# Kernel tuning notes

Measured on AMD Instinct MI355X. Metric: run time of the kernel, lower is better.

## Reference

```python
import jax, jax.numpy as jnp
import numpy as np

N_NODES = 100000
N_EDGES = 1600000
NFEAT, NHID, NCLASS = 512, 128, 64


def setup_inputs() -> dict:
    key = jax.random.key(0)
    ks = jax.random.split(key, 8)
    y = jax.random.normal(ks[0], (N_NODES, NFEAT), dtype=jnp.float32)
    src = jax.random.randint(ks[1], (N_EDGES,), 0, N_NODES, dtype=jnp.int64)
    dst = jax.random.randint(ks[2], (N_EDGES,), 0, N_NODES, dtype=jnp.int64)
    edge_w = jax.random.uniform(ks[3], (N_EDGES,), dtype=jnp.float32)
    # GraphConvolution params (Glorot-ish scale)
    W1 = jax.random.normal(ks[4], (NFEAT, NHID), dtype=jnp.float32) / np.sqrt(NFEAT)
    b1 = jax.random.normal(ks[5], (NHID,), dtype=jnp.float32) * 0.01
    W2 = jax.random.normal(ks[6], (NHID, NCLASS), dtype=jnp.float32) / np.sqrt(NHID)
    b2 = jax.random.normal(ks[7], (NCLASS,), dtype=jnp.float32) * 0.01
    return {"y": y, "src": src, "dst": dst, "edge_w": edge_w,
            "W1": W1, "b1": b1, "W2": W2, "b2": b2}


def _graph_conv(x, W, b, src, dst, edge_w, n_nodes):
    # support = x @ W ; out = spmm(adj, support) + b  (adj in COO form)
    support = x @ W                                   # [N, out_dim]
    msgs = support[src] * edge_w[:, None]             # [E, out_dim] gather
    agg = jax.ops.segment_sum(msgs, dst, num_segments=n_nodes)  # scatter-add
    return agg + b


def reference(y, src, dst, edge_w, W1, b1, W2, b2):
    h = jax.nn.leaky_relu(_graph_conv(y, W1, b1, src, dst, edge_w, N_NODES),
                          negative_slope=0.01)        # F.leaky_relu default
    y_embedding = h
    logits = _graph_conv(h, W2, b2, src, dst, edge_w, N_NODES)
    return (jax.nn.softmax(logits, axis=1), y_embedding)
```

## Files before the change

kernel.cpp:

```cpp
#include <hip/hip_runtime.h>
#include <hip/hip_fp16.h>

#define NN 100000
#define NE 1600000
#define F0 512
#define F1 128
#define F2 64

typedef short bf16x8 __attribute__((ext_vector_type(8)));
typedef float f32x4  __attribute__((ext_vector_type(4)));

static __device__ __forceinline__ unsigned short f2bf(float f) {
    unsigned int u = __float_as_uint(f);
    return (unsigned short)((u + 0x7FFFu + ((u >> 16) & 1u)) >> 16);
}

static __device__ __forceinline__ unsigned short f2h(float f) {
    __half h = __float2half(f);
    return *(unsigned short*)&h;
}

static __device__ __forceinline__ float2 h2f2(unsigned int u) {
    __half2 h = *(__half2*)&u;
    return __half22float2(h);
}

__global__ __launch_bounds__(256)
void wt_kernel(const float* __restrict__ W1, const float* __restrict__ W2,
               unsigned short* __restrict__ W1t, unsigned short* __restrict__ W2t,
               int* __restrict__ cnt, int grid_threads)
{
    int i = blockIdx.x * 256 + threadIdx.x;
    if (i < F0 * F1) {
        int n = i / F0, k = i % F0;
        W1t[i] = f2bf(W1[k * F1 + n]);
    } else {
        int j = i - F0 * F1;
        if (j < F1 * F2) {
            int n = j / F1, k = j % F1;
            W2t[j] = f2bf(W2[k * F2 + n]);
        }
    }
    for (int z = i; z < NN + 256; z += grid_threads) cnt[z] = 0;
}

template<int BM, int BN, int BK, int TN, bool FILL>
__global__ __launch_bounds__(256)
void gemm_edge_kernel(const float* __restrict__ A, const unsigned short* __restrict__ Bt,
                      unsigned short* __restrict__ C, int M, int K, int N,
                      int row_base, int gemm_blocks,
                      const int* __restrict__ src, const int* __restrict__ dst,
                      const float* __restrict__ ew, const int* __restrict__ rowptr,
                      const int* __restrict__ bsum,
                      int* __restrict__ cnt, int* __restrict__ rank,
                      int2* __restrict__ rec, int ne)
{
    constexpr int LDA = BK + 8;
    constexpr int LDB = BK + 8;
    __shared__ unsigned short As[BM * LDA];
    __shared__ unsigned short Bs[BN * LDB];

    if ((int)blockIdx.x >= gemm_blocks) {
        int e = ((int)blockIdx.x - gemm_blocks) * 256 + threadIdx.x;
        if (e < ne) {
            if constexpr (!FILL) {
                rank[e] = atomicAdd(&cnt[dst[e]], 1);
            } else {
                int d = dst[e];
                int pos = rowptr[d] + bsum[d >> 8] + rank[e];
                rec[pos] = make_int2(src[e], __float_as_int(ew[e]));
            }
        }
        return;
    }

    const int tid  = threadIdx.x;
    const int wave = tid >> 6;
    const int lane = tid & 63;
    const int lr   = lane & 15;
    const int quad = lane >> 4;
    const int row0 = row_base + (int)blockIdx.x * BM;

    f32x4 acc[2][TN];
#pragma unroll
    for (int i = 0; i < 2; i++)
#pragma unroll
        for (int j = 0; j < TN; j++) acc[i][j] = (f32x4)0.f;

    for (int k0 = 0; k0 < K; k0 += BK) {
#pragma unroll
        for (int l = tid; l < BM * (BK / 4); l += 256) {
            int m  = l / (BK / 4);
            int kq = l % (BK / 4);
            int rg = row0 + m; if (rg >= M) rg = M - 1;
            float4 v = *(const float4*)(A + (long long)rg * K + k0 + kq * 4);
            ushort4 b = make_ushort4(f2bf(v.x), f2bf(v.y), f2bf(v.z), f2bf(v.w));
            *(ushort4*)(&As[m * LDA + kq * 4]) = b;
        }
#pragma unroll
        for (int l = tid; l < BN * (BK / 8); l += 256) {
            int n  = l / (BK / 8);
            int ko = l % (BK / 8);
            uint4 v = *(const uint4*)(Bt + (long long)n * K + k0 + ko * 8);
            *(uint4*)(&Bs[n * LDB + ko * 8]) = v;
        }
        __syncthreads();

#pragma unroll
        for (int kk = 0; kk < BK; kk += 32) {
            bf16x8 a[2], b[TN];
#pragma unroll
            for (int tm = 0; tm < 2; tm++)
                a[tm] = *(const bf16x8*)(&As[(wave * 32 + tm * 16 + lr) * LDA + kk + quad * 8]);
#pragma unroll
            for (int tn = 0; tn < TN; tn++)
                b[tn] = *(const bf16x8*)(&Bs[(tn * 16 + lr) * LDB + kk + quad * 8]);
#pragma unroll
            for (int tm = 0; tm < 2; tm++)
#pragma unroll
                for (int tn = 0; tn < TN; tn++)
                    acc[tm][tn] = __builtin_amdgcn_mfma_f32_16x16x32_bf16(
                        a[tm], b[tn], acc[tm][tn], 0, 0, 0);
        }
        __syncthreads();
    }

#pragma unroll
    for (int tm = 0; tm < 2; tm++) {
#pragma unroll
        for (int r = 0; r < 4; r++) {
            int row = row0 + wave * 32 + tm * 16 + quad * 4 + r;
            if (row < M) {
#pragma unroll
                for (int tn = 0; tn < TN; tn++)
                    C[(long long)row * N + tn * 16 + lr] = f2h(acc[tm][tn][r]);
            }
        }
    }
}

__global__ __launch_bounds__(256)
void scan1_kernel(const int* __restrict__ cnt, int* __restrict__ rowptr,
                  int* __restrict__ bsum, int n)
{
    __shared__ int s[256];
    int t = threadIdx.x;
    int i = blockIdx.x * 256 + t;
    int v = (i <= n) ? cnt[i] : 0;
    s[t] = v;
    __syncthreads();
#pragma unroll
    for (int off = 1; off < 256; off <<= 1) {
        int x = (t >= off) ? s[t - off] : 0;
        __syncthreads();
        s[t] += x;
        __syncthreads();
    }
    if (i <= n) rowptr[i] = s[t] - v;
    if (t == 255) bsum[blockIdx.x] = s[255];
}

__global__ __launch_bounds__(512)
void scan2_kernel(int* __restrict__ bsum, int nb)
{
    __shared__ int s[512];
    int t = threadIdx.x;
    int v = (t < nb) ? bsum[t] : 0;
    s[t] = v;
    __syncthreads();
#pragma unroll
    for (int off = 1; off < 512; off <<= 1) {
        int x = (t >= off) ? s[t - off] : 0;
        __syncthreads();
        s[t] += x;
        __syncthreads();
    }
    if (t < nb) bsum[t] = s[t] - v;
}

__global__ __launch_bounds__(256)
void agg1_fused_kernel(const unsigned int* __restrict__ sup, const int2* __restrict__ rec,
                       const int* __restrict__ rowptr, const int* __restrict__ bsum,
                       const float* __restrict__ b1,
                       const unsigned short* __restrict__ W2t,
                       float* __restrict__ h, unsigned short* __restrict__ sup2, int n)
{
    constexpr int LDH = F1 + 8;
    __shared__ unsigned short hsb[16 * LDH];

    const int tid  = threadIdx.x;
    const int w    = tid >> 6;
    const int lane = tid & 63;
    const int half = lane >> 5;
    const int sl   = lane & 31;
    const int base = blockIdx.x * 16;

    float4 bb = *(const float4*)(b1 + sl * 4);

#pragma unroll
    for (int it = 0; it < 2; it++) {
        int row  = w * 4 + it * 2 + half;
        int node = base + row;
        float4 acc = make_float4(0.f, 0.f, 0.f, 0.f);
        if (node < n) {
            int j   = rowptr[node]     + bsum[node >> 8];
            int end = rowptr[node + 1] + bsum[(node + 1) >> 8];
            for (; j + 8 <= end; j += 8) {
                int2 r[8];
#pragma unroll
                for (int u = 0; u < 8; u++) r[u] = rec[j + u];
                uint2 uu[8];
#pragma unroll
                for (int u = 0; u < 8; u++)
                    uu[u] = *(const uint2*)(&sup[(long long)r[u].x * 64 + sl * 2]);
#pragma unroll
                for (int u = 0; u < 8; u++) {
                    float2 fa = h2f2(uu[u].x);
                    float2 fb = h2f2(uu[u].y);
                    float  ww = __int_as_float(r[u].y);
                    acc.x = fmaf(fa.x, ww, acc.x);
                    acc.y = fmaf(fa.y, ww, acc.y);
                    acc.z = fmaf(fb.x, ww, acc.z);
                    acc.w = fmaf(fb.y, ww, acc.w);
                }
            }
            for (; j < end; j++) {
                int2 r0 = rec[j];
                uint2 u0 = *(const uint2*)(&sup[(long long)r0.x * 64 + sl * 2]);
                float2 fa = h2f2(u0.x);
                float2 fb = h2f2(u0.y);
                float  ww = __int_as_float(r0.y);
                acc.x = fmaf(fa.x, ww, acc.x);
                acc.y = fmaf(fa.y, ww, acc.y);
                acc.z = fmaf(fb.x, ww, acc.z);
                acc.w = fmaf(fb.y, ww, acc.w);
            }
            acc.x += bb.x;  acc.y += bb.y;  acc.z += bb.z;  acc.w += bb.w;
            acc.x = acc.x > 0.f ? acc.x : 0.01f * acc.x;
            acc.y = acc.y > 0.f ? acc.y : 0.01f * acc.y;
            acc.z = acc.z > 0.f ? acc.z : 0.01f * acc.z;
            acc.w = acc.w > 0.f ? acc.w : 0.01f * acc.w;
            *(float4*)(h + (long long)node * 128 + sl * 4) = acc;
        }
        ushort4 hv = (node < n)
            ? make_ushort4(f2bf(acc.x), f2bf(acc.y), f2bf(acc.z), f2bf(acc.w))
            : make_ushort4(0, 0, 0, 0);
        *(ushort4*)(&hsb[row * LDH + sl * 4]) = hv;
    }
    __syncthreads();

    const int lr   = lane & 15;
    const int quad = lane >> 4;
    f32x4 acc2 = (f32x4)0.f;
#pragma unroll
    for (int kk = 0; kk < F1; kk += 32) {
        bf16x8 a = *(const bf16x8*)(&hsb[lr * LDH + kk + quad * 8]);
        bf16x8 b = *(const bf16x8*)(W2t + (w * 16 + lr) * F1 + kk + quad * 8);
        acc2 = __builtin_amdgcn_mfma_f32_16x16x32_bf16(a, b, acc2, 0, 0, 0);
    }
#pragma unroll
    for (int r = 0; r < 4; r++) {
        int node = base + quad * 4 + r;
        if (node < n)
            sup2[(long long)node * 64 + w * 16 + lr] = f2h(acc2[r]);
    }
}

__global__ __launch_bounds__(256)
void agg2_kernel(const unsigned short* __restrict__ sup, const int2* __restrict__ rec,
                 const int* __restrict__ rowptr, const int* __restrict__ bsum,
                 const float* __restrict__ b2, float* __restrict__ out, int n)
{
    const int lane = threadIdx.x & 63;
    const int half = lane >> 5;
    const int sl   = lane & 31;
    const int node = blockIdx.x * 8 + (threadIdx.x >> 6) * 2 + half;
    if (node >= n) return;

    int j   = rowptr[node]     + bsum[node >> 8];
    int end = rowptr[node + 1] + bsum[(node + 1) >> 8];
    float2 acc = make_float2(0.f, 0.f);

    for (; j + 8 <= end; j += 8) {
        int2 r[8];
#pragma unroll
        for (int u = 0; u < 8; u++) r[u] = rec[j + u];
        unsigned int uu[8];
#pragma unroll
        for (int u = 0; u < 8; u++)
            uu[u] = *(const unsigned int*)(&sup[(long long)r[u].x * 64 + sl * 2]);
#pragma unroll
        for (int u = 0; u < 8; u++) {
            float2 f = h2f2(uu[u]);
            float  ww = __int_as_float(r[u].y);
            acc.x = fmaf(f.x, ww, acc.x);
            acc.y = fmaf(f.y, ww, acc.y);
        }
    }
    for (; j < end; j++) {
        int2 r0 = rec[j];
        unsigned int u0 = *(const unsigned int*)(&sup[(long long)r0.x * 64 + sl * 2]);
        float2 f = h2f2(u0);
        float  ww = __int_as_float(r0.y);
        acc.x = fmaf(f.x, ww, acc.x);
        acc.y = fmaf(f.y, ww, acc.y);
    }

    float2 bv = *(const float2*)(b2 + sl * 2);
    float2 v  = make_float2(acc.x + bv.x, acc.y + bv.y);
    float m = fmaxf(v.x, v.y);
#pragma unroll
    for (int off = 16; off; off >>= 1) m = fmaxf(m, __shfl_xor(m, off, 64));
    float2 e = make_float2(__expf(v.x - m), __expf(v.y - m));
    float s = e.x + e.y;
#pragma unroll
    for (int off = 16; off; off >>= 1) s += __shfl_xor(s, off, 64);
    float inv = 1.f / s;
    *(float2*)(out + (long long)node * 64 + sl * 2) = make_float2(e.x * inv, e.y * inv);
}

extern "C" void kernel_launch(void* const* d_in, const int* in_sizes, int n_in,
                              void* d_out, int out_size, void* d_ws, size_t ws_size,
                              hipStream_t stream)
{
    const float* y   = (const float*)d_in[0];
    const int*   src = (const int*)  d_in[1];
    const int*   dst = (const int*)  d_in[2];
    const float* ew  = (const float*)d_in[3];
    const float* W1  = (const float*)d_in[4];
    const float* b1  = (const float*)d_in[5];
    const float* W2  = (const float*)d_in[6];
    const float* b2  = (const float*)d_in[7];

    float* out     = (float*)d_out;
    float* softout = out;
    float* h       = out + (size_t)NN * F2;

    char* ws = (char*)d_ws;
    size_t o = 0;
    auto alloc = [&](size_t bytes) -> void* {
        void* p = ws + o;
        o = (o + bytes + 255) & ~(size_t)255;
        return p;
    };
    unsigned short* sup  = (unsigned short*)alloc((size_t)NN * F1 * 2);
    unsigned short* sup2 = (unsigned short*)alloc((size_t)NN * F2 * 2);
    int2*           rec  = (int2*)          alloc((size_t)NE * 8);
    int*            rank = (int*)           alloc((size_t)NE * 4);
    int*            rowptr = (int*)         alloc((size_t)(NN + 2) * 4);
    int*            cnt  = (int*)           alloc((size_t)(NN + 256) * 4);
    int*            bsum = (int*)           alloc(512 * 4);
    unsigned short* W1t  = (unsigned short*)alloc((size_t)F0 * F1 * 2);
    unsigned short* W2t  = (unsigned short*)alloc((size_t)F1 * F2 * 2);

    const int NB = (NN + 255) / 256;
    const int GB = (NN + 127) / 128;
    const int GA = 312;
    const int EB = (NE + 255) / 256;

    wt_kernel<<<NB, 256, 0, stream>>>(W1, W2, W1t, W2t, cnt, NB * 256);

    gemm_edge_kernel<128, 128, 64, 8, false><<<GA + EB, 256, 0, stream>>>(
        y, W1t, sup, NN, F0, F1, 0, GA,
        src, dst, ew, rowptr, bsum, cnt, rank, rec, NE);

    scan1_kernel<<<NB, 256, 0, stream>>>(cnt, rowptr, bsum, NN);
    scan2_kernel<<<1, 512, 0, stream>>>(bsum, NB);

    gemm_edge_kernel<128, 128, 64, 8, true><<<(GB - GA) + EB, 256, 0, stream>>>(
        y, W1t, sup, NN, F0, F1, GA * 128, GB - GA,
        src, dst, ew, rowptr, bsum, cnt, rank, rec, NE);

    agg1_fused_kernel<<<(NN + 15) / 16, 256, 0, stream>>>(
        (const unsigned int*)sup, rec, rowptr, bsum, b1, W2t, h, sup2, NN);

    agg2_kernel<<<(NN + 7) / 8, 256, 0, stream>>>(
        sup2, rec, rowptr, bsum, b2, softout, NN);
}
```

Before: 553.2 us.

## Overlap scan with GEMM tiles and use nontemporal loads/stores for streaming data

Moves 64 GEMM row-tiles into the scan1 launch so the prefix-scan blocks share a grid with GEMM blocks, which fills the otherwise small scan launch with useful work and shrinks the final GEMM+fill launch. The GEMM body is factored into a shared device helper. Edge records, rank, the h output and the softmax output now go through nontemporal loads and stores, so these single-use streams are meant to stay out of cache and leave room for the gathered support rows. The combined kernel's shared-memory footprint is the GEMM's, which may limit occupancy for the scan blocks.

```diff
diff --git a/kernel.cpp b/kernel.cpp
--- a/kernel.cpp
+++ b/kernel.cpp
@@ -9,6 +9,7 @@
 
 typedef short bf16x8 __attribute__((ext_vector_type(8)));
 typedef float f32x4  __attribute__((ext_vector_type(4)));
+typedef float f32x2  __attribute__((ext_vector_type(2)));
 
 static __device__ __forceinline__ unsigned short f2bf(float f) {
     unsigned int u = __float_as_uint(f);
@@ -42,6 +43,79 @@
         }
     }
     for (int z = i; z < NN + 256; z += grid_threads) cnt[z] = 0;
+}
+
+template<int BM, int BN, int BK, int TN>
+static __device__ __forceinline__
+void gemm_tile(unsigned short* As, unsigned short* Bs,
+               const float* __restrict__ A, const unsigned short* __restrict__ Bt,
+               unsigned short* __restrict__ C, int M, int K, int N, int row0)
+{
+    constexpr int LDA = BK + 8;
+    constexpr int LDB = BK + 8;
+
+    const int tid  = threadIdx.x;
+    const int wave = tid >> 6;
+    const int lane = tid & 63;
+    const int lr   = lane & 15;
+    const int quad = lane >> 4;
+
+    f32x4 acc[2][TN];
+#pragma unroll
+    for (int i = 0; i < 2; i++)
+#pragma unroll
+        for (int j = 0; j < TN; j++) acc[i][j] = (f32x4)0.f;
+
+    for (int k0 = 0; k0 < K; k0 += BK) {
+#pragma unroll
+        for (int l = tid; l < BM * (BK / 4); l += 256) {
+            int m  = l / (BK / 4);
+            int kq = l % (BK / 4);
+            int rg = row0 + m; if (rg >= M) rg = M - 1;
+            float4 v = *(const float4*)(A + (long long)rg * K + k0 + kq * 4);
+            ushort4 b = make_ushort4(f2bf(v.x), f2bf(v.y), f2bf(v.z), f2bf(v.w));
+            *(ushort4*)(&As[m * LDA + kq * 4]) = b;
+        }
+#pragma unroll
+        for (int l = tid; l < BN * (BK / 8); l += 256) {
+            int n  = l / (BK / 8);
+            int ko = l % (BK / 8);
+            uint4 v = *(const uint4*)(Bt + (long long)n * K + k0 + ko * 8);
+            *(uint4*)(&Bs[n * LDB + ko * 8]) = v;
+        }
+        __syncthreads();
+
+#pragma unroll
+        for (int kk = 0; kk < BK; kk += 32) {
+            bf16x8 a[2], b[TN];
+#pragma unroll
+            for (int tm = 0; tm < 2; tm++)
+                a[tm] = *(const bf16x8*)(&As[(wave * 32 + tm * 16 + lr) * LDA + kk + quad * 8]);
+#pragma unroll
+            for (int tn = 0; tn < TN; tn++)
+                b[tn] = *(const bf16x8*)(&Bs[(tn * 16 + lr) * LDB + kk + quad * 8]);
+#pragma unroll
+            for (int tm = 0; tm < 2; tm++)
+#pragma unroll
+                for (int tn = 0; tn < TN; tn++)
+                    acc[tm][tn] = __builtin_amdgcn_mfma_f32_16x16x32_bf16(
+                        a[tm], b[tn], acc[tm][tn], 0, 0, 0);
+        }
+        __syncthreads();
+    }
+
+#pragma unroll
+    for (int tm = 0; tm < 2; tm++) {
+#pragma unroll
+        for (int r = 0; r < 4; r++) {
+            int row = row0 + wave * 32 + tm * 16 + quad * 4 + r;
+            if (row < M) {
+#pragma unroll
+                for (int tn = 0; tn < TN; tn++)
+                    C[(long long)row * N + tn * 16 + lr] = f2h(acc[tm][tn][r]);
+            }
+        }
+    }
 }
 
 template<int BM, int BN, int BK, int TN, bool FILL>
@@ -55,109 +129,60 @@
                       int* __restrict__ cnt, int* __restrict__ rank,
                       int2* __restrict__ rec, int ne)
 {
-    constexpr int LDA = BK + 8;
-    constexpr int LDB = BK + 8;
-    __shared__ unsigned short As[BM * LDA];
-    __shared__ unsigned short Bs[BN * LDB];
+    __shared__ unsigned short As[BM * (BK + 8)];
+    __shared__ unsigned short Bs[BN * (BK + 8)];
 
     if ((int)blockIdx.x >= gemm_blocks) {
         int e = ((int)blockIdx.x - gemm_blocks) * 256 + threadIdx.x;
         if (e < ne) {
             if constexpr (!FILL) {
-                rank[e] = atomicAdd(&cnt[dst[e]], 1);
+                int rk = atomicAdd(&cnt[dst[e]], 1);
+                __builtin_nontemporal_store(rk, &rank[e]);
             } else {
                 int d = dst[e];
-                int pos = rowptr[d] + bsum[d >> 8] + rank[e];
+                int rk = __builtin_nontemporal_load(&rank[e]);
+                int pos = rowptr[d] + bsum[d >> 8] + rk;
                 rec[pos] = make_int2(src[e], __float_as_int(ew[e]));
             }
         }
         return;
     }
-
-    const int tid  = threadIdx.x;
-    const int wave = tid >> 6;
-    const int lane = tid & 63;
-    const int lr   = lane & 15;
-    const int quad = lane >> 4;
-    const int row0 = row_base + (int)blockIdx.x * BM;
-
-    f32x4 acc[2][TN];
-#pragma unroll
-    for (int i = 0; i < 2; i++)
-#pragma unroll
-        for (int j = 0; j < TN; j++) acc[i][j] = (f32x4)0.f;
-
-    for (int k0 = 0; k0 < K; k0 += BK) {
-#pragma unroll
-        for (int l = tid; l < BM * (BK / 4); l += 256) {
-            int m  = l / (BK / 4);
-            int kq = l % (BK / 4);
-            int rg = row0 + m; if (rg >= M) rg = M - 1;
-            float4 v = *(const float4*)(A + (long long)rg * K + k0 + kq * 4);
-            ushort4 b = make_ushort4(f2bf(v.x), f2bf(v.y), f2bf(v.z), f2bf(v.w));
-            *(ushort4*)(&As[m * LDA + kq * 4]) = b;
-        }
-#pragma unroll
-        for (int l = tid; l < BN * (BK / 8); l += 256) {
-            int n  = l / (BK / 8);
-            int ko = l % (BK / 8);
-            uint4 v = *(const uint4*)(Bt + (long long)n * K + k0 + ko * 8);
-            *(uint4*)(&Bs[n * LDB + ko * 8]) = v;
-        }
+    gemm_tile<BM, BN, BK, TN>(As, Bs, A, Bt, C, M, K, N,
+                              row_base + (int)blockIdx.x * BM);
+}
+
+template<int BM, int BN, int BK, int TN>
+__global__ __launch_bounds__(256)
+void gemm_scan_kernel(const float* __restrict__ A, const unsigned short* __restrict__ Bt,
+                      unsigned short* __restrict__ C, int M, int K, int N,
+                      int row_base, int gemm_blocks,
+                      const int* __restrict__ cnt, int* __restrict__ rowptr,
+                      int* __restrict__ bsum, int n)
+{
+    __shared__ unsigned short As[BM * (BK + 8)];
+    __shared__ unsigned short Bs[BN * (BK + 8)];
+
+    if ((int)blockIdx.x >= gemm_blocks) {
+        __shared__ int s[256];
+        int blk = (int)blockIdx.x - gemm_blocks;
+        int t = threadIdx.x;
+        int i = blk * 256 + t;
+        int v = (i <= n) ? cnt[i] : 0;
+        s[t] = v;
         __syncthreads();
-
-#pragma unroll
-        for (int kk = 0; kk < BK; kk += 32) {
-            bf16x8 a[2], b[TN];
-#pragma unroll
-            for (int tm = 0; tm < 2; tm++)
-                a[tm] = *(const bf16x8*)(&As[(wave * 32 + tm * 16 + lr) * LDA + kk + quad * 8]);
-#pragma unroll
-            for (int tn = 0; tn < TN; tn++)
-                b[tn] = *(const bf16x8*)(&Bs[(tn * 16 + lr) * LDB + kk + quad * 8]);
-#pragma unroll
-            for (int tm = 0; tm < 2; tm++)
-#pragma unroll
-                for (int tn = 0; tn < TN; tn++)
-                    acc[tm][tn] = __builtin_amdgcn_mfma_f32_16x16x32_bf16(
-                        a[tm], b[tn], acc[tm][tn], 0, 0, 0);
-        }
-        __syncthreads();
-    }
-
-#pragma unroll
-    for (int tm = 0; tm < 2; tm++) {
-#pragma unroll
-        for (int r = 0; r < 4; r++) {
-            int row = row0 + wave * 32 + tm * 16 + quad * 4 + r;
-            if (row < M) {
-#pragma unroll
-                for (int tn = 0; tn < TN; tn++)
-                    C[(long long)row * N + tn * 16 + lr] = f2h(acc[tm][tn][r]);
-            }
-        }
-    }
-}
-
-__global__ __launch_bounds__(256)
-void scan1_kernel(const int* __restrict__ cnt, int* __restrict__ rowptr,
-                  int* __restrict__ bsum, int n)
-{
-    __shared__ int s[256];
-    int t = threadIdx.x;
-    int i = blockIdx.x * 256 + t;
-    int v = (i <= n) ? cnt[i] : 0;
-    s[t] = v;
-    __syncthreads();
-#pragma unroll
-    for (int off = 1; off < 256; off <<= 1) {
-        int x = (t >= off) ? s[t - off] : 0;
-        __syncthreads();
-        s[t] += x;
-        __syncthreads();
-    }
-    if (i <= n) rowptr[i] = s[t] - v;
-    if (t == 255) bsum[blockIdx.x] = s[255];
+#pragma unroll
+        for (int off = 1; off < 256; off <<= 1) {
+            int x = (t >= off) ? s[t - off] : 0;
+            __syncthreads();
+            s[t] += x;
+            __syncthreads();
+        }
+        if (i <= n) rowptr[i] = s[t] - v;
+        if (t == 255) bsum[blk] = s[255];
+        return;
+    }
+    gemm_tile<BM, BN, BK, TN>(As, Bs, A, Bt, C, M, K, N,
+                              row_base + (int)blockIdx.x * BM);
 }
 
 __global__ __launch_bounds__(512)
@@ -188,6 +213,8 @@
     constexpr int LDH = F1 + 8;
     __shared__ unsigned short hsb[16 * LDH];
 
+    const long long* recq = (const long long*)rec;
+
     const int tid  = threadIdx.x;
     const int w    = tid >> 6;
     const int lane = tid & 63;
@@ -195,29 +222,29 @@
     const int sl   = lane & 31;
     const int base = blockIdx.x * 16;
 
-    float4 bb = *(const float4*)(b1 + sl * 4);
+    f32x4 bb = *(const f32x4*)(b1 + sl * 4);
 
 #pragma unroll
     for (int it = 0; it < 2; it++) {
         int row  = w * 4 + it * 2 + half;
         int node = base + row;
-        float4 acc = make_float4(0.f, 0.f, 0.f, 0.f);
+        f32x4 acc = (f32x4)0.f;
         if (node < n) {
             int j   = rowptr[node]     + bsum[node >> 8];
             int end = rowptr[node + 1] + bsum[(node + 1) >> 8];
             for (; j + 8 <= end; j += 8) {
-                int2 r[8];
-#pragma unroll
-                for (int u = 0; u < 8; u++) r[u] = rec[j + u];
+                long long r[8];
+#pragma unroll
+                for (int u = 0; u < 8; u++) r[u] = __builtin_nontemporal_load(&recq[j + u]);
                 uint2 uu[8];
 #pragma unroll
                 for (int u = 0; u < 8; u++)
-                    uu[u] = *(const uint2*)(&sup[(long long)r[u].x * 64 + sl * 2]);
+                    uu[u] = *(const uint2*)(&sup[(long long)(int)r[u] * 64 + sl * 2]);
 #pragma unroll
                 for (int u = 0; u < 8; u++) {
                     float2 fa = h2f2(uu[u].x);
                     float2 fb = h2f2(uu[u].y);
-                    float  ww = __int_as_float(r[u].y);
+                    float  ww = __int_as_float((int)(r[u] >> 32));
                     acc.x = fmaf(fa.x, ww, acc.x);
                     acc.y = fmaf(fa.y, ww, acc.y);
                     acc.z = fmaf(fb.x, ww, acc.z);
@@ -225,11 +252,11 @@
                 }
             }
             for (; j < end; j++) {
-                int2 r0 = rec[j];
-                uint2 u0 = *(const uint2*)(&sup[(long long)r0.x * 64 + sl * 2]);
+                long long r0 = __builtin_nontemporal_load(&recq[j]);
+                uint2 u0 = *(const uint2*)(&sup[(long long)(int)r0 * 64 + sl * 2]);
                 float2 fa = h2f2(u0.x);
                 float2 fb = h2f2(u0.y);
-                float  ww = __int_as_float(r0.y);
+                float  ww = __int_as_float((int)(r0 >> 32));
                 acc.x = fmaf(fa.x, ww, acc.x);
                 acc.y = fmaf(fa.y, ww, acc.y);
                 acc.z = fmaf(fb.x, ww, acc.z);
@@ -240,7 +267,7 @@
             acc.y = acc.y > 0.f ? acc.y : 0.01f * acc.y;
             acc.z = acc.z > 0.f ? acc.z : 0.01f * acc.z;
             acc.w = acc.w > 0.f ? acc.w : 0.01f * acc.w;
-            *(float4*)(h + (long long)node * 128 + sl * 4) = acc;
+            __builtin_nontemporal_store(acc, (f32x4*)(h + (long long)node * 128 + sl * 4));
         }
         ushort4 hv = (node < n)
             ? make_ushort4(f2bf(acc.x), f2bf(acc.y), f2bf(acc.z), f2bf(acc.w))
@@ -271,6 +298,7 @@
                  const int* __restrict__ rowptr, const int* __restrict__ bsum,
                  const float* __restrict__ b2, float* __restrict__ out, int n)
 {
+    const long long* recq = (const long long*)rec;
     const int lane = threadIdx.x & 63;
     const int half = lane >> 5;
     const int sl   = lane & 31;
@@ -282,26 +310,26 @@
     float2 acc = make_float2(0.f, 0.f);
 
     for (; j + 8 <= end; j += 8) {
-        int2 r[8];
-#pragma unroll
-        for (int u = 0; u < 8; u++) r[u] = rec[j + u];
+        long long r[8];
+#pragma unroll
+        for (int u = 0; u < 8; u++) r[u] = __builtin_nontemporal_load(&recq[j + u]);
         unsigned int uu[8];
 #pragma unroll
         for (int u = 0; u < 8; u++)
-            uu[u] = *(const unsigned int*)(&sup[(long long)r[u].x * 64 + sl * 2]);
+            uu[u] = *(const unsigned int*)(&sup[(long long)(int)r[u] * 64 + sl * 2]);
 #pragma unroll
         for (int u = 0; u < 8; u++) {
             float2 f = h2f2(uu[u]);
-            float  ww = __int_as_float(r[u].y);
+            float  ww = __int_as_float((int)(r[u] >> 32));
             acc.x = fmaf(f.x, ww, acc.x);
             acc.y = fmaf(f.y, ww, acc.y);
         }
     }
     for (; j < end; j++) {
-        int2 r0 = rec[j];
-        unsigned int u0 = *(const unsigned int*)(&sup[(long long)r0.x * 64 + sl * 2]);
+        long long r0 = __builtin_nontemporal_load(&recq[j]);
+        unsigned int u0 = *(const unsigned int*)(&sup[(long long)(int)r0 * 64 + sl * 2]);
         float2 f = h2f2(u0);
-        float  ww = __int_as_float(r0.y);
+        float  ww = __int_as_float((int)(r0 >> 32));
         acc.x = fmaf(f.x, ww, acc.x);
         acc.y = fmaf(f.y, ww, acc.y);
     }
@@ -316,7 +344,8 @@
 #pragma unroll
     for (int off = 16; off; off >>= 1) s += __shfl_xor(s, off, 64);
     float inv = 1.f / s;
-    *(float2*)(out + (long long)node * 64 + sl * 2) = make_float2(e.x * inv, e.y * inv);
+    f32x2 r; r.x = e.x * inv; r.y = e.y * inv;
+    __builtin_nontemporal_store(r, (f32x2*)(out + (long long)node * 64 + sl * 2));
 }
 
 extern "C" void kernel_launch(void* const* d_in, const int* in_sizes, int n_in,
@@ -356,6 +385,8 @@
     const int NB = (NN + 255) / 256;
     const int GB = (NN + 127) / 128;
     const int GA = 312;
+    const int GS = 64;
+    const int GC = GB - GA - GS;
     const int EB = (NE + 255) / 256;
 
     wt_kernel<<<NB, 256, 0, stream>>>(W1, W2, W1t, W2t, cnt, NB * 256);
@@ -364,11 +395,14 @@
         y, W1t, sup, NN, F0, F1, 0, GA,
         src, dst, ew, rowptr, bsum, cnt, rank, rec, NE);
 
-    scan1_kernel<<<NB, 256, 0, stream>>>(cnt, rowptr, bsum, NN);
+    gemm_scan_kernel<128, 128, 64, 8><<<GS + NB, 256, 0, stream>>>(
+        y, W1t, sup, NN, F0, F1, GA * 128, GS,
+        cnt, rowptr, bsum, NN);
+
     scan2_kernel<<<1, 512, 0, stream>>>(bsum, NB);
 
-    gemm_edge_kernel<128, 128, 64, 8, true><<<(GB - GA) + EB, 256, 0, stream>>>(
-        y, W1t, sup, NN, F0, F1, GA * 128, GB - GA,
+    gemm_edge_kernel<128, 128, 64, 8, true><<<GC + EB, 256, 0, stream>>>(
+        y, W1t, sup, NN, F0, F1, (GA + GS) * 128, GC,
         src, dst, ew, rowptr, bsum, cnt, rank, rec, NE);
 
     agg1_fused_kernel<<<(NN + 15) / 16, 256, 0, stream>>>(
```

New measurement: 608.3 us. 10.0% more time.
